# Optimization experiments

Measured on AMD Instinct MI355X. Metric: run time of the kernel, lower is better.

The kernel has to match this reference:

```python
import jax, jax.numpy as jnp
import numpy as np

B, N, D, OUT, NUM_ITERS = 8, 4096, 1024, 1024, 3
LN_EPS = 1e-5


def setup_inputs() -> dict:
    key = jax.random.key(0)
    ks = jax.random.split(key, 8)
    s = (6.0 / (2 * D)) ** 0.5  # xavier-uniform-like scale
    return {
        "query": jax.random.normal(ks[0], (B, D), jnp.float32),
        "feat": jax.random.normal(ks[1], (B, N, D), jnp.float32),
        "W_h": jax.random.uniform(ks[2], (D, D), jnp.float32, -s, s),
        "W_f": jax.random.uniform(ks[3], (D, D), jnp.float32, -s, s),
        "W_g": jax.random.normal(ks[4], (4, D, D), jnp.float32) / np.sqrt(D),
        "ln_w": jnp.ones((D,), jnp.float32),
        "ln_b": jnp.zeros((D,), jnp.float32),
        "W_out": jax.random.uniform(ks[5], (OUT, D), jnp.float32, -s, s),
        "b_out": jnp.zeros((OUT,), jnp.float32),
        "feat_mask": jax.random.bernoulli(ks[6], 0.2, (B, 1, 1, N)),
    }


def _layer_norm(x, w, b):
    mu = x.mean(-1, keepdims=True)
    var = jnp.var(x, axis=-1, keepdims=True)
    return (x - mu) / jnp.sqrt(var + LN_EPS) * w + b


def reference(query, feat, W_h, W_f, W_g, ln_w, ln_b, W_out, b_out, feat_mask):
    q = query @ W_h                       # [B, D]
    f = feat @ W_f                        # [B, N, D]
    mask = feat_mask.reshape(feat.shape[0], feat.shape[1])  # squeeze(1).squeeze(1)
    b = jnp.where(mask, jnp.float32(-1e18), jnp.float32(0.0))  # [B, N]
    # feat_group is iteration-invariant: mean over the 4 orthogonal transforms
    # mean_g(f @ W_g[g].T) == f @ mean_g(W_g).T
    fg = f @ W_g.mean(0).T                # [B, N, D]
    n = fg.shape[1]
    for i in range(NUM_ITERS):
        c = jax.nn.softmax(b, axis=1)     # [B, N]
        if i == NUM_ITERS - 1:
            out = jnp.einsum('bn,bnd->bd', c, fg)
        else:
            delta = jnp.einsum('bd,bnd->bn', q, fg)
            delta = (delta - delta.mean(1, keepdims=True)) / (
                delta.std(1, keepdims=True, ddof=1) + 1e-9)  # torch.std is unbiased
            b = b + delta
            out = jnp.einsum('bn,bnd->bd', c, fg) / n  # mean over dim 1
        q = _layer_norm(q + jax.nn.selu(out), ln_w, ln_b)
    return q @ W_out.T + b_out
```

## Files before the change

kernel.cpp:

```cpp
#include <hip/hip_runtime.h>
#include <hip/hip_bf16.h>


using u16 = unsigned short;
using u32 = unsigned int;
using u8  = unsigned char;
using u64 = unsigned long long;

#define SELU_L 1.0507009873554805f
#define SELU_A 1.6732632423543772f

__device__ float g_M[1048576];
__device__ float g_Q[1048576];
__device__ float g_Qt[1048576];
__device__ float g_q[8192];
__device__ float g_q2[8192];
__device__ float g_s[8192];
__device__ float g_bst[32768];
__device__ float g_c[32768];
__device__ float g_delta[32768];
__device__ float g_outv[8192];
__device__ float g_v[8192];
__device__ int   g_dt[12];

__device__ __forceinline__ float blo(u32 u){ return __uint_as_float(u << 16); }
__device__ __forceinline__ float bhi(u32 u){ return __uint_as_float(u & 0xffff0000u); }
__device__ __forceinline__ float b2f(u16 u){ return __uint_as_float(((u32)u) << 16); }

__device__ __forceinline__ void unpack8(uint4 x, float* f){
  f[0]=blo(x.x); f[1]=bhi(x.x); f[2]=blo(x.y); f[3]=bhi(x.y);
  f[4]=blo(x.z); f[5]=bhi(x.z); f[6]=blo(x.w); f[7]=bhi(x.w);
}

__device__ __forceinline__ float ldf(const void* p, size_t i, int dt){
  return dt ? ((const float*)p)[i] : b2f(((const u16*)p)[i]);
}
__device__ __forceinline__ void load8(const void* base, size_t idx, int dt, float* f){
  if (dt == 0) {
    uint4 x = *(const uint4*)((const u16*)base + idx);
    unpack8(x, f);
  } else {
    const float* p = (const float*)base + idx;
    float4 a = *(const float4*)p, b = *(const float4*)(p + 4);
    f[0]=a.x; f[1]=a.y; f[2]=a.z; f[3]=a.w; f[4]=b.x; f[5]=b.y; f[6]=b.z; f[7]=b.w;
  }
}

__device__ __forceinline__ float wredsum(float x){
#pragma unroll
  for (int o = 32; o; o >>= 1) x += __shfl_xor(x, o, 64);
  return x;
}

__global__ void kdet(const void* p0, const void* p1, const void* p2, const void* p3,
                     const void* p4, const void* p5, const void* p6, const void* p7,
                     const void* p8, const void* p9)
{
  const void* ps[10] = {p0,p1,p2,p3,p4,p5,p6,p7,p8,p9};
  int tid = threadIdx.x;
  int w = tid >> 6, lane = tid & 63;
  if (w < 9) {
    const u16* wp = (const u16*)ps[w];
    u16 x0 = wp[lane], x1 = wp[64 + lane];
    int e0 = (x0 >> 7) & 0xFF, e1 = (x1 >> 7) & 0xFF;
    u64 nz0 = __ballot(x0 != 0), nz1 = __ballot(x1 != 0);
    u64 pa0 = __ballot(x0 != 0 && e0 >= 0x70 && e0 <= 0x8F);
    u64 pa1 = __ballot(x1 != 0 && e1 >= 0x70 && e1 <= 0x8F);
    if (lane == 0) {
      const u64 evenm = 0x5555555555555555ULL;
      int nz = __popcll(nz0) + __popcll(nz1);
      int pass = __popcll(pa0) + __popcll(pa1);
      int evenNZ = __popcll(nz0 & evenm) + __popcll(nz1 & evenm);
      int oddNZ  = nz - evenNZ;
      int dt;
      if (nz == 0)                    dt = 0;
      else if (evenNZ == 0 && oddNZ)  dt = 1;
      else                            dt = (pass * 10 >= nz * 9) ? 0 : 1;
      g_dt[w] = dt;
    }
  } else if (w == 9) {
    const u8* mp = (const u8*)ps[9];
    u64 v = ((const u64*)mp)[lane];
    bool f16c=false, isF=false, nz01=false, nzNon4=false, nzM8_4=false, anynz=false;
#pragma unroll
    for (int j = 0; j < 8; ++j) {
      u8 cb = (u8)(v >> (8 * j));
      if (!cb) continue;
      int i = lane * 8 + j;
      anynz = true;
      if (cb == 0x3C && (i & 1)) f16c = true;
      if (cb == 0x3F || cb == 0x80) isF = true;
      int m = i & 3;
      if (m == 0 || m == 1) nz01 = true;
      if (m != 0) nzNon4 = true;
      if ((i & 7) == 4) nzM8_4 = true;
    }
    bool A  = __ballot(f16c)   != 0;
    bool Bf = __ballot(isF)    != 0;
    bool C  = __ballot(nz01)   != 0;
    bool Dn = __ballot(nzNon4) != 0;
    bool E  = __ballot(nzM8_4) != 0;
    bool F  = __ballot(anynz)  != 0;
    if (lane == 0) {
      int mode;
      if (A)       mode = 4;
      else if (Bf) mode = C ? 2 : 3;
      else if (Dn) mode = 0;
      else if (E)  mode = 1;
      else if (F)  mode = 5;
      else         mode = 1;
      g_dt[9] = mode;
    }
  }
  for (int i = tid; i < 8192; i += 640) g_q[i] = 0.f;
}

__global__ void kprep(const void* __restrict__ Wg, const void* __restrict__ Wh,
                      const void* __restrict__ query, const u8* __restrict__ maskp)
{
  int blk = blockIdx.x, tid = threadIdx.x;
  if (blk < 1024) {
    int dtg = g_dt[4];
    int e = blk * 1024 + tid * 4;
    float a0=0.f,a1=0.f,a2=0.f,a3=0.f;
#pragma unroll
    for (int g = 0; g < 4; ++g) {
      size_t o = (size_t)g * 1048576 + e;
      a0 += ldf(Wg, o+0, dtg); a1 += ldf(Wg, o+1, dtg);
      a2 += ldf(Wg, o+2, dtg); a3 += ldf(Wg, o+3, dtg);
    }
    *(float4*)(g_M + e) = make_float4(a0*0.25f, a1*0.25f, a2*0.25f, a3*0.25f);
  } else if (blk < 1088) {
    int dtq = g_dt[0], dth = g_dt[2];
    __shared__ float ql[512];
    int blk2 = blk - 1024;
    int kt = blk2 & 3, dc = blk2 >> 2;
    for (int idx = tid; idx < 512; idx += 256) {
      int b = idx >> 6, d = idx & 63;
      ql[idx] = ldf(query, b * 1024 + dc * 64 + d, dtq);
    }
    __syncthreads();
    int k = kt * 256 + tid;
    float acc[8] = {0,0,0,0,0,0,0,0};
    for (int dd = 0; dd < 64; ++dd) {
      int d = dc * 64 + dd;
      float w = ldf(Wh, (size_t)d * 1024 + k, dth);
#pragma unroll
      for (int b = 0; b < 8; ++b) acc[b] += ql[(b << 6) + dd] * w;
    }
#pragma unroll
    for (int b = 0; b < 8; ++b) atomicAdd(&g_q[b * 1024 + k], acc[b]);
  } else {
    int mode = g_dt[9];
    int e0 = (blk - 1088) * 1024 + tid * 4;
#pragma unroll
    for (int j = 0; j < 4; ++j) {
      int e = e0 + j;
      bool on;
      if (mode == 0)      on = maskp[e] != 0;
      else if (mode == 1) on = ((const int*)maskp)[e] != 0;
      else if (mode == 2) on = ((const u16*)maskp)[e] != 0;
      else if (mode == 3) on = ((const u32*)maskp)[e] != 0;
      else if (mode == 4) on = ((const u16*)maskp)[e] != 0;
      else                on = ((const u64*)maskp)[e] != 0ULL;
      g_bst[e] = on ? -1e18f : 0.f;
    }
  }
}

__global__ void __launch_bounds__(256) kq_mat(const void* __restrict__ Wf)
{
  __shared__ float As[64 * 65];
  __shared__ float Bs[64 * 65];
  int tid = threadIdx.x;
  int k0 = (blockIdx.x & 15) * 64, d0 = (blockIdx.x >> 4) * 64;
  int dtf = g_dt[3];
  int tx = tid & 15, ty = tid >> 4;
  float acc[4][4];
#pragma unroll
  for (int i = 0; i < 4; ++i)
#pragma unroll
    for (int l = 0; l < 4; ++l) acc[i][l] = 0.f;

  for (int jc = 0; jc < 1024; jc += 64) {
    if (jc) __syncthreads();
#pragma unroll
    for (int t2 = 0; t2 < 2; ++t2) {
      int idx = tid + t2 * 256;
      int row = idx >> 3, seg = idx & 7;
      float f[8];
      load8(Wf, (size_t)(k0 + row) * 1024 + jc + seg * 8, dtf, f);
#pragma unroll
      for (int u = 0; u < 8; ++u) As[row * 65 + seg * 8 + u] = f[u];
      const float* mrow = g_M + (size_t)(d0 + row) * 1024 + jc + seg * 8;
      float4 m0 = *(const float4*)mrow, m1 = *(const float4*)(mrow + 4);
      Bs[row * 65 + seg * 8 + 0] = m0.x; Bs[row * 65 + seg * 8 + 1] = m0.y;
      Bs[row * 65 + seg * 8 + 2] = m0.z; Bs[row * 65 + seg * 8 + 3] = m0.w;
      Bs[row * 65 + seg * 8 + 4] = m1.x; Bs[row * 65 + seg * 8 + 5] = m1.y;
      Bs[row * 65 + seg * 8 + 6] = m1.z; Bs[row * 65 + seg * 8 + 7] = m1.w;
    }
    __syncthreads();
#pragma unroll 8
    for (int j = 0; j < 64; ++j) {
      float a0 = As[(ty * 4 + 0) * 65 + j];
      float a1 = As[(ty * 4 + 1) * 65 + j];
      float a2 = As[(ty * 4 + 2) * 65 + j];
      float a3 = As[(ty * 4 + 3) * 65 + j];
      float b0 = Bs[(tx * 4 + 0) * 65 + j];
      float b1 = Bs[(tx * 4 + 1) * 65 + j];
      float b2 = Bs[(tx * 4 + 2) * 65 + j];
      float b3 = Bs[(tx * 4 + 3) * 65 + j];
      acc[0][0] += a0*b0; acc[0][1] += a0*b1; acc[0][2] += a0*b2; acc[0][3] += a0*b3;
      acc[1][0] += a1*b0; acc[1][1] += a1*b1; acc[1][2] += a1*b2; acc[1][3] += a1*b3;
      acc[2][0] += a2*b0; acc[2][1] += a2*b1; acc[2][2] += a2*b2; acc[2][3] += a2*b3;
      acc[3][0] += a3*b0; acc[3][1] += a3*b1; acc[3][2] += a3*b2; acc[3][3] += a3*b3;
    }
  }
#pragma unroll
  for (int i = 0; i < 4; ++i) {
    *(float4*)(g_Q + (size_t)(k0 + ty * 4 + i) * 1024 + d0 + tx * 4) =
        make_float4(acc[i][0], acc[i][1], acc[i][2], acc[i][3]);
  }
  __syncthreads();
#pragma unroll
  for (int i = 0; i < 4; ++i)
#pragma unroll
    for (int l = 0; l < 4; ++l) As[(tx * 4 + l) * 65 + ty * 4 + i] = acc[i][l];
  __syncthreads();
  {
    int row = tid >> 2, q4 = tid & 3;
    float v16[16];
#pragma unroll
    for (int e = 0; e < 16; ++e) v16[e] = As[row * 65 + q4 * 16 + e];
#pragma unroll
    for (int c2 = 0; c2 < 4; ++c2)
      *(float4*)(g_Qt + (size_t)(d0 + row) * 1024 + k0 + q4 * 16 + c2 * 4) =
          make_float4(v16[c2*4], v16[c2*4+1], v16[c2*4+2], v16[c2*4+3]);
  }
}

__device__ __forceinline__ void build_ql(float* ql, const float* qsrc, float scale,
                                         const void* lnw, const void* lnb, int tid)
{
  int w = tid >> 6, lane = tid & 63;
  int dtw = g_dt[5], dtb = g_dt[6];
#pragma unroll
  for (int rr = 0; rr < 2; ++rr) {
    int b = w + rr * 4;
    const float* qb = qsrc + b * 1024;
    const float* ob = g_outv + b * 1024;
    float x[16]; float sum = 0.f, sq = 0.f;
#pragma unroll
    for (int cc = 0; cc < 4; ++cc) {
      float4 qv = *(const float4*)(qb + cc * 256 + lane * 4);
      float4 ov = *(const float4*)(ob + cc * 256 + lane * 4);
      float q4[4] = {qv.x, qv.y, qv.z, qv.w};
      float o4[4] = {ov.x, ov.y, ov.z, ov.w};
#pragma unroll
      for (int e = 0; e < 4; ++e) {
        float o = o4[e] * scale;
        float se = (o > 0.f) ? SELU_L * o : SELU_L * SELU_A * expm1f(o);
        float val = q4[e] + se;
        x[cc * 4 + e] = val; sum += val; sq += val * val;
      }
    }
    sum = wredsum(sum); sq = wredsum(sq);
    float mean = sum * (1.f / 1024.f);
    float var = fmaxf(sq * (1.f / 1024.f) - mean * mean, 0.f);
    float rstd = rsqrtf(var + 1e-5f);
#pragma unroll
    for (int cc = 0; cc < 4; ++cc)
#pragma unroll
      for (int e = 0; e < 4; ++e) {
        int d = cc * 256 + lane * 4 + e;
        ql[b * 1024 + d] = (x[cc * 4 + e] - mean) * rstd * ldf(lnw, d, dtw)
                           + ldf(lnb, d, dtb);
      }
  }
  __syncthreads();
}

__global__ void __launch_bounds__(256) kmerge(const void* __restrict__ lnw,
                                              const void* __restrict__ lnb,
                                              int phase, float scale)
{
  int blk = blockIdx.x, tid = threadIdx.x;
  if (blk < 8) {
    __shared__ float sm[1024];
    int b = blk;
    const float* row = g_bst + b * 4096;
    float mx = -3.4e38f;
    for (int i = tid; i < 4096; i += 256) mx = fmaxf(mx, row[i]);
    sm[tid] = mx; __syncthreads();
    for (int s2 = 128; s2; s2 >>= 1) { if (tid < s2) sm[tid] = fmaxf(sm[tid], sm[tid + s2]); __syncthreads(); }
    mx = sm[0]; __syncthreads();
    float sum = 0.f;
    for (int i = tid; i < 4096; i += 256) {
      float e = __expf(row[i] - mx);
      g_c[b * 4096 + i] = e; sum += e;
    }
    sm[tid] = sum; __syncthreads();
    for (int s2 = 128; s2; s2 >>= 1) { if (tid < s2) sm[tid] += sm[tid + s2]; __syncthreads(); }
    float inv = 1.f / sm[0];
    for (int i = tid; i < 4096; i += 256) g_c[b * 4096 + i] *= inv;
    for (int i = tid; i < 1024; i += 256) g_s[b * 1024 + i] = 0.f;
    return;
  }
  __shared__ float ql[8192];
  const float* qsrc = (phase == 2) ? g_q2 : g_q;
  if (phase == 0) {
    for (int i = tid; i < 8192; i += 256) ql[i] = qsrc[i];
    __syncthreads();
  } else {
    build_ql(ql, qsrc, scale, lnw, lnb, tid);
  }
  if (phase >= 1 && blk == 8) {
    float* qdst = (phase == 2) ? g_q : g_q2;
    for (int i = tid; i < 8192; i += 256) qdst[i] = ql[i];
  }
  if (phase == 2) return;
  int w = tid >> 6, lane = tid & 63;
  int k = (blk - 8) * 4 + w;
  const float* Qrow = g_Q + (size_t)k * 1024;
  float f[16];
#pragma unroll
  for (int cc = 0; cc < 4; ++cc) {
    float4 x = *(const float4*)(Qrow + cc * 256 + lane * 4);
    f[cc*4] = x.x; f[cc*4+1] = x.y; f[cc*4+2] = x.z; f[cc*4+3] = x.w;
  }
  float acc[8];
#pragma unroll
  for (int b = 0; b < 8; ++b) {
    const float* qb = ql + b * 1024;
    float d = 0.f;
#pragma unroll
    for (int cc = 0; cc < 4; ++cc) {
      float4 qv = *(const float4*)(qb + cc * 256 + lane * 4);
      d += f[cc*4] * qv.x + f[cc*4+1] * qv.y + f[cc*4+2] * qv.z + f[cc*4+3] * qv.w;
    }
    acc[b] = wredsum(d);
  }
  if (lane == 0) {
#pragma unroll
    for (int b = 0; b < 8; ++b) g_v[b * 1024 + k] = acc[b];
  }
}

__global__ void __launch_bounds__(256)
kfeat(const void* __restrict__ feat, int need_delta)
{
  __shared__ float sl[4][1024];
  int tid = threadIdx.x, w = tid >> 6, lane = tid & 63;
  int b = blockIdx.x >> 6, ch = blockIdx.x & 63;
  int dtf = g_dt[1];
  float vr[16];
#pragma unroll
  for (int j = 0; j < 16; ++j) vr[j] = 0.f;
  if (need_delta) {
    const float* vb = g_v + b * 1024;
#pragma unroll
    for (int j = 0; j < 8; ++j) { vr[j] = vb[lane * 8 + j]; vr[8 + j] = vb[512 + lane * 8 + j]; }
  }
  int n0 = ch * 64 + w * 16;
  float cc16[16];
#pragma unroll
  for (int r = 0; r < 16; ++r) cc16[r] = g_c[b * 4096 + n0 + r];
  float acc[16];
#pragma unroll
  for (int j = 0; j < 16; ++j) acc[j] = 0.f;
  float dp[16];
  for (int r = 0; r < 16; ++r) {
    size_t row = ((size_t)b * 4096 + n0 + r) * 1024;
    float f[16];
    load8(feat, row + lane * 8, dtf, f);
    load8(feat, row + 512 + lane * 8, dtf, f + 8);
    float cn = cc16[r];
#pragma unroll
    for (int j = 0; j < 16; ++j) acc[j] += cn * f[j];
    float dot = 0.f;
    if (need_delta) {
#pragma unroll
      for (int j = 0; j < 16; ++j) dot += f[j] * vr[j];
    }
    dp[r] = dot;
  }
  if (need_delta) {
#pragma unroll
    for (int r = 0; r < 16; ++r) dp[r] = wredsum(dp[r]);
    if (lane == 0) {
#pragma unroll
      for (int r = 0; r < 16; ++r) g_delta[b * 4096 + n0 + r] = dp[r];
    }
  }
#pragma unroll
  for (int j = 0; j < 8; ++j) {
    sl[w][lane * 8 + j] = acc[j];
    sl[w][512 + lane * 8 + j] = acc[8 + j];
  }
  __syncthreads();
#pragma unroll
  for (int j = 0; j < 4; ++j) {
    int k = tid * 4 + j;
    float val = sl[0][k] + sl[1][k] + sl[2][k] + sl[3][k];
    atomicAdd(&g_s[b * 1024 + k], val);
  }
}

__global__ void __launch_bounds__(256) kpost(int do_stats)
{
  __shared__ float sh[8192];
  int blk = blockIdx.x, tid = threadIdx.x;
  if (blk < 8) {
    if (!do_stats) return;
    int b = blk;
    const float* row = g_delta + b * 4096;
    float xs[16], sum = 0.f, sq = 0.f;
#pragma unroll
    for (int r = 0; r < 16; ++r) { float x = row[tid + 256 * r]; xs[r] = x; sum += x; sq += x * x; }
    sh[tid] = sum; __syncthreads();
    for (int s2 = 128; s2; s2 >>= 1) { if (tid < s2) sh[tid] += sh[tid + s2]; __syncthreads(); }
    sum = sh[0]; __syncthreads();
    sh[tid] = sq; __syncthreads();
    for (int s2 = 128; s2; s2 >>= 1) { if (tid < s2) sh[tid] += sh[tid + s2]; __syncthreads(); }
    sq = sh[0];
    float mean = sum / 4096.f;
    float var = fmaxf((sq - 4096.f * mean * mean) / 4095.f, 0.f);
    float inv = 1.f / (sqrtf(var) + 1e-9f);
#pragma unroll
    for (int r = 0; r < 16; ++r) {
      int i = tid + 256 * r;
      g_bst[b * 4096 + i] += (xs[r] - mean) * inv;
    }
    return;
  }
  for (int i = tid; i < 8192; i += 256) sh[i] = g_s[i];
  __syncthreads();
  int w = tid >> 6, lane = tid & 63;
  int d = (blk - 8) * 4 + w;
  const float* Qtr = g_Qt + (size_t)d * 1024;
  float f[16];
#pragma unroll
  for (int cc = 0; cc < 4; ++cc) {
    float4 x = *(const float4*)(Qtr + cc * 256 + lane * 4);
    f[cc*4] = x.x; f[cc*4+1] = x.y; f[cc*4+2] = x.z; f[cc*4+3] = x.w;
  }
  float acc[8];
#pragma unroll
  for (int b = 0; b < 8; ++b) {
    const float* sb = sh + b * 1024;
    float dd = 0.f;
#pragma unroll
    for (int cc = 0; cc < 4; ++cc) {
      float4 sv = *(const float4*)(sb + cc * 256 + lane * 4);
      dd += f[cc*4] * sv.x + f[cc*4+1] * sv.y + f[cc*4+2] * sv.z + f[cc*4+3] * sv.w;
    }
    acc[b] = wredsum(dd);
  }
  if (lane == 0) {
#pragma unroll
    for (int b = 0; b < 8; ++b) g_outv[b * 1024 + d] = acc[b];
  }
}

__global__ void __launch_bounds__(256) kfin(const void* __restrict__ Wout,
                                            const void* __restrict__ bout,
                                            const void* __restrict__ lnw,
                                            const void* __restrict__ lnb,
                                            float* __restrict__ out)
{
  __shared__ float ql[8192];
  int tid = threadIdx.x;
  build_ql(ql, g_q, 1.f, lnw, lnb, tid);
  int w = tid >> 6, lane = tid & 63;
  int o = blockIdx.x * 4 + w;
  int dto = g_dt[7], dtb = g_dt[8];
  size_t row = (size_t)o * 1024;
  float f[16];
  load8(Wout, row + lane * 8, dto, f);
  load8(Wout, row + 512 + lane * 8, dto, f + 8);
  float acc[8];
#pragma unroll
  for (int b = 0; b < 8; ++b) {
    const float* qb = ql + b * 1024;
    float d = 0.f;
#pragma unroll
    for (int j = 0; j < 8; ++j) d += f[j]     * qb[lane * 8 + j];
#pragma unroll
    for (int j = 0; j < 8; ++j) d += f[8 + j] * qb[512 + lane * 8 + j];
    acc[b] = wredsum(d);
  }
  if (lane == 0) {
    float bo = ldf(bout, o, dtb);
#pragma unroll
    for (int b = 0; b < 8; ++b) out[b * 1024 + o] = acc[b] + bo;
  }
}

extern "C" void kernel_launch(void* const* d_in, const int* in_sizes, int n_in,
                              void* d_out, int out_size, void* d_ws, size_t ws_size,
                              hipStream_t stream)
{
  const void* query = d_in[0];
  const void* feat  = d_in[1];
  const void* Wh    = d_in[2];
  const void* Wf    = d_in[3];
  const void* Wg    = d_in[4];
  const void* lnw   = d_in[5];
  const void* lnb   = d_in[6];
  const void* Wout  = d_in[7];
  const void* bout  = d_in[8];
  const u8*   maskp = (const u8*)d_in[9];
  (void)in_sizes; (void)n_in; (void)out_size; (void)d_ws; (void)ws_size;

  kdet<<<1, 640, 0, stream>>>(query, feat, Wh, Wf, Wg, lnw, lnb, Wout, bout, maskp);
  kprep<<<1120, 256, 0, stream>>>(Wg, Wh, query, maskp);
  kq_mat<<<256, 256, 0, stream>>>(Wf);

  for (int i = 0; i < 3; ++i) {
    int nl = (i < 2);
    kmerge<<<(i == 2) ? 9 : 264, 256, 0, stream>>>(lnw, lnb, i, 1.f / 4096.f);
    kfeat<<<512, 256, 0, stream>>>(feat, nl);
    kpost<<<264, 256, 0, stream>>>(nl);
  }
  kfin<<<256, 256, 0, stream>>>(Wout, bout, lnw, lnb, (float*)d_out);
}
```

Before: 458.9 us.

## Split-K the Q matrix product with atomics and move transpose into merge kernel

The 1024x1024x1024 product that builds Q now runs as 1024 blocks, each covering a quarter of the reduction dimension, and accumulates into Q with atomicAdd after kprep zeroes it. Shared tiles are stored transposed with a padded stride of 68 so the inner loop can use float4 shared-memory reads. Writing the transposed copy Qt moves out of the GEMM into extra blocks of the first merge launch. The goal is to fill the device better than the old 256-block launch allowed. The cost is many atomic operations and an extra read pass over Q, and float summation order is no longer deterministic.

Result: no change. 467.7 us (+1.9%).

```diff
diff --git a/kernel.cpp b/kernel.cpp
--- a/kernel.cpp
+++ b/kernel.cpp
@@ -150,7 +150,7 @@
     }
 #pragma unroll
     for (int b = 0; b < 8; ++b) atomicAdd(&g_q[b * 1024 + k], acc[b]);
-  } else {
+  } else if (blk < 1120) {
     int mode = g_dt[9];
     int e0 = (blk - 1088) * 1024 + tid * 4;
 #pragma unroll
@@ -165,78 +165,69 @@
       else                on = ((const u64*)maskp)[e] != 0ULL;
       g_bst[e] = on ? -1e18f : 0.f;
     }
+  } else {
+    int base = (blk - 1120) * 4096 + tid * 4;
+    float4 z = make_float4(0.f, 0.f, 0.f, 0.f);
+#pragma unroll
+    for (int it = 0; it < 4; ++it) *(float4*)(g_Q + base + it * 1024) = z;
   }
 }
 
 __global__ void __launch_bounds__(256) kq_mat(const void* __restrict__ Wf)
 {
-  __shared__ float As[64 * 65];
-  __shared__ float Bs[64 * 65];
+  __shared__ float As[64 * 68];
+  __shared__ float Bs[64 * 68];
   int tid = threadIdx.x;
-  int k0 = (blockIdx.x & 15) * 64, d0 = (blockIdx.x >> 4) * 64;
+  int t = blockIdx.x & 255, split = blockIdx.x >> 8;
+  int k0 = (t & 15) * 64, d0 = (t >> 4) * 64;
+  int j0 = split * 256;
   int dtf = g_dt[3];
   int tx = tid & 15, ty = tid >> 4;
+  int s = tid & 3, r = tid >> 2;
   float acc[4][4];
 #pragma unroll
-  for (int i = 0; i < 4; ++i)
-#pragma unroll
-    for (int l = 0; l < 4; ++l) acc[i][l] = 0.f;
-
-  for (int jc = 0; jc < 1024; jc += 64) {
-    if (jc) __syncthreads();
-#pragma unroll
-    for (int t2 = 0; t2 < 2; ++t2) {
-      int idx = tid + t2 * 256;
-      int row = idx >> 3, seg = idx & 7;
+  for (int i2 = 0; i2 < 4; ++i2)
+#pragma unroll
+    for (int l = 0; l < 4; ++l) acc[i2][l] = 0.f;
+
+  for (int jc = j0; jc < j0 + 256; jc += 64) {
+    if (jc != j0) __syncthreads();
+    {
       float f[8];
-      load8(Wf, (size_t)(k0 + row) * 1024 + jc + seg * 8, dtf, f);
-#pragma unroll
-      for (int u = 0; u < 8; ++u) As[row * 65 + seg * 8 + u] = f[u];
-      const float* mrow = g_M + (size_t)(d0 + row) * 1024 + jc + seg * 8;
-      float4 m0 = *(const float4*)mrow, m1 = *(const float4*)(mrow + 4);
-      Bs[row * 65 + seg * 8 + 0] = m0.x; Bs[row * 65 + seg * 8 + 1] = m0.y;
-      Bs[row * 65 + seg * 8 + 2] = m0.z; Bs[row * 65 + seg * 8 + 3] = m0.w;
-      Bs[row * 65 + seg * 8 + 4] = m1.x; Bs[row * 65 + seg * 8 + 5] = m1.y;
-      Bs[row * 65 + seg * 8 + 6] = m1.z; Bs[row * 65 + seg * 8 + 7] = m1.w;
+      size_t wrow = (size_t)(k0 + r) * 1024 + jc + s * 16;
+      load8(Wf, wrow, dtf, f);
+#pragma unroll
+      for (int u = 0; u < 8; ++u) As[(s * 16 + u) * 68 + r] = f[u];
+      load8(Wf, wrow + 8, dtf, f);
+#pragma unroll
+      for (int u = 0; u < 8; ++u) As[(s * 16 + 8 + u) * 68 + r] = f[u];
+      const float* mrow = g_M + (size_t)(d0 + r) * 1024 + jc + s * 16;
+      float4 m0 = ((const float4*)mrow)[0], m1 = ((const float4*)mrow)[1];
+      float4 m2 = ((const float4*)mrow)[2], m3 = ((const float4*)mrow)[3];
+      float g[16] = {m0.x,m0.y,m0.z,m0.w, m1.x,m1.y,m1.z,m1.w,
+                     m2.x,m2.y,m2.z,m2.w, m3.x,m3.y,m3.z,m3.w};
+#pragma unroll
+      for (int u = 0; u < 16; ++u) Bs[(s * 16 + u) * 68 + r] = g[u];
     }
     __syncthreads();
 #pragma unroll 8
     for (int j = 0; j < 64; ++j) {
-      float a0 = As[(ty * 4 + 0) * 65 + j];
-      float a1 = As[(ty * 4 + 1) * 65 + j];
-      float a2 = As[(ty * 4 + 2) * 65 + j];
-      float a3 = As[(ty * 4 + 3) * 65 + j];
-      float b0 = Bs[(tx * 4 + 0) * 65 + j];
-      float b1 = Bs[(tx * 4 + 1) * 65 + j];
-      float b2 = Bs[(tx * 4 + 2) * 65 + j];
-      float b3 = Bs[(tx * 4 + 3) * 65 + j];
-      acc[0][0] += a0*b0; acc[0][1] += a0*b1; acc[0][2] += a0*b2; acc[0][3] += a0*b3;
-      acc[1][0] += a1*b0; acc[1][1] += a1*b1; acc[1][2] += a1*b2; acc[1][3] += a1*b3;
-      acc[2][0] += a2*b0; acc[2][1] += a2*b1; acc[2][2] += a2*b2; acc[2][3] += a2*b3;
-      acc[3][0] += a3*b0; acc[3][1] += a3*b1; acc[3][2] += a3*b2; acc[3][3] += a3*b3;
-    }
-  }
-#pragma unroll
-  for (int i = 0; i < 4; ++i) {
-    *(float4*)(g_Q + (size_t)(k0 + ty * 4 + i) * 1024 + d0 + tx * 4) =
-        make_float4(acc[i][0], acc[i][1], acc[i][2], acc[i][3]);
-  }
-  __syncthreads();
-#pragma unroll
-  for (int i = 0; i < 4; ++i)
-#pragma unroll
-    for (int l = 0; l < 4; ++l) As[(tx * 4 + l) * 65 + ty * 4 + i] = acc[i][l];
-  __syncthreads();
-  {
-    int row = tid >> 2, q4 = tid & 3;
-    float v16[16];
-#pragma unroll
-    for (int e = 0; e < 16; ++e) v16[e] = As[row * 65 + q4 * 16 + e];
-#pragma unroll
-    for (int c2 = 0; c2 < 4; ++c2)
-      *(float4*)(g_Qt + (size_t)(d0 + row) * 1024 + k0 + q4 * 16 + c2 * 4) =
-          make_float4(v16[c2*4], v16[c2*4+1], v16[c2*4+2], v16[c2*4+3]);
-  }
+      float4 av = *(const float4*)(As + j * 68 + ty * 4);
+      float4 bv = *(const float4*)(Bs + j * 68 + tx * 4);
+      float a4[4] = {av.x, av.y, av.z, av.w};
+      float b4[4] = {bv.x, bv.y, bv.z, bv.w};
+#pragma unroll
+      for (int i2 = 0; i2 < 4; ++i2)
+#pragma unroll
+        for (int l = 0; l < 4; ++l) acc[i2][l] += a4[i2] * b4[l];
+    }
+  }
+#pragma unroll
+  for (int i2 = 0; i2 < 4; ++i2)
+#pragma unroll
+    for (int l = 0; l < 4; ++l)
+      atomicAdd(&g_Q[(size_t)(k0 + ty * 4 + i2) * 1024 + d0 + tx * 4 + l],
+                acc[i2][l]);
 }
 
 __device__ __forceinline__ void build_ql(float* ql, const float* qsrc, float scale,
@@ -284,6 +275,7 @@
                                               const void* __restrict__ lnb,
                                               int phase, float scale)
 {
+  __shared__ float ql[8192];
   int blk = blockIdx.x, tid = threadIdx.x;
   if (blk < 8) {
     __shared__ float sm[1024];
@@ -306,7 +298,27 @@
     for (int i = tid; i < 1024; i += 256) g_s[b * 1024 + i] = 0.f;
     return;
   }
-  __shared__ float ql[8192];
+  if (phase == 0 && blk >= 264) {
+    int t = blk - 264;
+    int k0 = (t & 15) * 64, d0 = (t >> 4) * 64;
+    int q4 = tid & 3, r = tid >> 2;
+    const float* src = g_Q + (size_t)(k0 + r) * 1024 + d0 + q4 * 16;
+    float4 v0 = ((const float4*)src)[0], v1 = ((const float4*)src)[1];
+    float4 v2 = ((const float4*)src)[2], v3 = ((const float4*)src)[3];
+    float vv[16] = {v0.x,v0.y,v0.z,v0.w, v1.x,v1.y,v1.z,v1.w,
+                    v2.x,v2.y,v2.z,v2.w, v3.x,v3.y,v3.z,v3.w};
+#pragma unroll
+    for (int u = 0; u < 16; ++u) ql[r * 65 + q4 * 16 + u] = vv[u];
+    __syncthreads();
+    float o[16];
+#pragma unroll
+    for (int u = 0; u < 16; ++u) o[u] = ql[(q4 * 16 + u) * 65 + r];
+    float* dst = g_Qt + (size_t)(d0 + r) * 1024 + k0 + q4 * 16;
+#pragma unroll
+    for (int c2 = 0; c2 < 4; ++c2)
+      *(float4*)(dst + c2 * 4) = make_float4(o[c2*4], o[c2*4+1], o[c2*4+2], o[c2*4+3]);
+    return;
+  }
   const float* qsrc = (phase == 2) ? g_q2 : g_q;
   if (phase == 0) {
     for (int i = tid; i < 8192; i += 256) ql[i] = qsrc[i];
@@ -513,12 +525,12 @@
   (void)in_sizes; (void)n_in; (void)out_size; (void)d_ws; (void)ws_size;
 
   kdet<<<1, 640, 0, stream>>>(query, feat, Wh, Wf, Wg, lnw, lnb, Wout, bout, maskp);
-  kprep<<<1120, 256, 0, stream>>>(Wg, Wh, query, maskp);
-  kq_mat<<<256, 256, 0, stream>>>(Wf);
+  kprep<<<1376, 256, 0, stream>>>(Wg, Wh, query, maskp);
+  kq_mat<<<1024, 256, 0, stream>>>(Wf);
 
   for (int i = 0; i < 3; ++i) {
     int nl = (i < 2);
-    kmerge<<<(i == 2) ? 9 : 264, 256, 0, stream>>>(lnw, lnb, i, 1.f / 4096.f);
+    kmerge<<<(i == 0) ? 520 : (nl ? 264 : 9), 256, 0, stream>>>(lnw, lnb, i, 1.f / 4096.f);
     kfeat<<<512, 256, 0, stream>>>(feat, nl);
     kpost<<<264, 256, 0, stream>>>(nl);
   }
```
